# Performance work log

Hardware: AMD Instinct MI355X
Metric: run time of the kernel (lower is better)

Reference implementation:

```python
import jax, jax.numpy as jnp
import numpy as np

D = 256
H = 16
HD = D // H
N_BIAS = 6
B, E = 8, 1024


def _layernorm(x, g, b, eps=1e-5):
    mu = jnp.mean(x, axis=-1, keepdims=True)
    var = jnp.mean(jnp.square(x - mu), axis=-1, keepdims=True)
    return (x - mu) * jax.lax.rsqrt(var + eps) * g + b


def setup_inputs() -> dict:
    key = jax.random.key(0)
    ks = jax.random.split(key, 16)
    s = 0.02
    inp = {
        "x": jax.random.normal(ks[0], (B, E, D), dtype=jnp.float32),
        "struct_bias": jax.random.randint(ks[1], (B, E, E), 0, N_BIAS),
        "key_padding_mask": jnp.zeros((B, E), dtype=bool),
        # projections stored as [in, out] so y = x @ W + b
        "Wq": jax.random.normal(ks[2], (D, D), jnp.float32) * s,
        "bq": jnp.zeros((D,), jnp.float32),
        "Wk": jax.random.normal(ks[3], (D, D), jnp.float32) * s,
        "bk": jnp.zeros((D,), jnp.float32),
        "Wv": jax.random.normal(ks[4], (D, D), jnp.float32) * s,
        "bv": jnp.zeros((D,), jnp.float32),
        "Wo": jax.random.normal(ks[5], (D, D), jnp.float32) * s,
        "bo": jnp.zeros((D,), jnp.float32),
        "bias_emb": jax.random.normal(ks[6], (N_BIAS, H), jnp.float32) * s,
        "ln1_g": jnp.ones((D,), jnp.float32),
        "ln1_b": jnp.zeros((D,), jnp.float32),
        "W_ff1": jax.random.normal(ks[7], (D, 4 * D), jnp.float32) * s,
        "b_ff1": jnp.zeros((4 * D,), jnp.float32),
        "W_ff2": jax.random.normal(ks[8], (4 * D, D), jnp.float32) * s,
        "b_ff2": jnp.zeros((D,), jnp.float32),
        "ln2_g": jnp.ones((D,), jnp.float32),
        "ln2_b": jnp.zeros((D,), jnp.float32),
    }
    return inp


def reference(x, struct_bias, key_padding_mask, Wq, bq, Wk, bk, Wv, bv, Wo, bo,
              bias_emb, ln1_g, ln1_b, W_ff1, b_ff1, W_ff2, b_ff2, ln2_g, ln2_b):
    b, e, d = x.shape
    # project and split heads: [B, H, E, HD]
    q = (x @ Wq + bq).reshape(b, e, H, HD).transpose(0, 2, 1, 3)
    k = (x @ Wk + bk).reshape(b, e, H, HD).transpose(0, 2, 1, 3)
    v = (x @ Wv + bv).reshape(b, e, H, HD).transpose(0, 2, 1, 3)
    scores = jnp.einsum('bhqd,bhkd->bhqk', q, k) / np.sqrt(HD).astype(np.float32)
    # learned structural bias: [B,E,E,H] -> [B,H,E,E]
    bias = bias_emb[struct_bias].transpose(0, 3, 1, 2)
    scores = scores + bias
    scores = jnp.where(key_padding_mask[:, None, None, :], -jnp.inf, scores)
    attn = jax.nn.softmax(scores, axis=-1)
    out = jnp.einsum('bhqk,bhkd->bhqd', attn, v)
    out = out.transpose(0, 2, 1, 3).reshape(b, e, d)
    out = out @ Wo + bo
    x = _layernorm(x + out, ln1_g, ln1_b)
    ff = jax.nn.gelu(x @ W_ff1 + b_ff1, approximate=False) @ W_ff2 + b_ff2
    x = _layernorm(x + ff, ln2_g, ln2_b)
    return x
```

## Files before the change

### kernel.cpp

```cpp
#include <hip/hip_runtime.h>
#include <math.h>

#define B_  8
#define E_  1024
#define D_  256
#define H_  16
#define FF_ 1024
#define M_  (B_ * E_)

typedef __attribute__((ext_vector_type(8))) short short8;
typedef __attribute__((ext_vector_type(4))) float f32x4;
typedef unsigned short bf16u;

#define GLOAD_LDS16(g, l) __builtin_amdgcn_global_load_lds( \
    (const __attribute__((address_space(1))) void*)(g), \
    (__attribute__((address_space(3))) void*)(l), 16, 0, 0)

__device__ __forceinline__ unsigned short f2bf(float f) {
  union { float f; unsigned u; } c; c.f = f;
  unsigned r = c.u + 0x7fffu + ((c.u >> 16) & 1u);
  return (unsigned short)(r >> 16);
}
__device__ __forceinline__ float gelu_exact(float x) {
  return 0.5f * x * (1.0f + erff(x * 0.70710678118654752f));
}

template<int BM, int BN, int EPI>
__global__ __launch_bounds__(256) void mm_k(
    const bf16u* __restrict__ A, const bf16u* __restrict__ Wt,
    const float* __restrict__ bias, const float* __restrict__ R,
    void* __restrict__ Cout, int M, int N, int K)
{
  constexpr int WM = BM / 2, WN = BN / 2;
  constexpr int MT = WM / 16, NT = WN / 16;
  constexpr int PA = BM * 8 / 256, PB = BN * 8 / 256;
  constexpr int LBM = (BM == 128 ? 7 : 6), LBN = (BN == 128 ? 7 : 6);
  __shared__ bf16u As[BM * 64];
  __shared__ bf16u Bs[BN * 64];

  const int t = threadIdx.x;
  const int l15 = t & 15, quad = (t >> 4) & 3;
  const int w = t >> 6, wm = w >> 1, wn = w & 1;
  const int m0 = blockIdx.x * BM, n0 = blockIdx.y * BN;

  f32x4 acc[MT][NT];
  const f32x4 z4 = {0.f, 0.f, 0.f, 0.f};
#pragma unroll
  for (int i = 0; i < MT; ++i)
#pragma unroll
    for (int j = 0; j < NT; ++j) acc[i][j] = z4;

  for (int k0 = 0; k0 < K; k0 += 64) {
    __syncthreads();
#pragma unroll
    for (int p = 0; p < PA; ++p) {
      int g = p * 256 + t;
      int m = g & (BM - 1), c = g >> LBM;
      const bf16u* src = A + (size_t)(m0 + m) * K + k0 + c * 8;
      GLOAD_LDS16(src, As + g * 8);
    }
#pragma unroll
    for (int p = 0; p < PB; ++p) {
      int g = p * 256 + t;
      int n = g & (BN - 1), c = g >> LBN;
      const bf16u* src = Wt + (size_t)(n0 + n) * K + k0 + c * 8;
      GLOAD_LDS16(src, Bs + g * 8);
    }
    __syncthreads();
#pragma unroll
    for (int s = 0; s < 2; ++s) {
      short8 af[MT], bfr[NT];
#pragma unroll
      for (int mt = 0; mt < MT; ++mt)
        af[mt] = *(const short8*)(As + ((s * 4 + quad) * BM + wm * WM + mt * 16 + l15) * 8);
#pragma unroll
      for (int nt = 0; nt < NT; ++nt)
        bfr[nt] = *(const short8*)(Bs + ((s * 4 + quad) * BN + wn * WN + nt * 16 + l15) * 8);
#pragma unroll
      for (int mt = 0; mt < MT; ++mt)
#pragma unroll
        for (int nt = 0; nt < NT; ++nt)
          acc[mt][nt] = __builtin_amdgcn_mfma_f32_16x16x32_bf16(
              af[mt], bfr[nt], acc[mt][nt], 0, 0, 0);
    }
  }

#pragma unroll
  for (int mt = 0; mt < MT; ++mt) {
#pragma unroll
    for (int nt = 0; nt < NT; ++nt) {
      int col = n0 + wn * WN + nt * 16 + l15;
      float bia = bias[col];
#pragma unroll
      for (int r = 0; r < 4; ++r) {
        int row = m0 + wm * WM + mt * 16 + quad * 4 + r;
        float v = acc[mt][nt][r] + bia;
        if (EPI == 3) {
          size_t pidx = ((((size_t)(row >> 10) * 16 + ((col >> 4) & 15)) * 3 +
                          (col >> 8)) * E_ + (row & 1023)) * 16 + (col & 15);
          ((bf16u*)Cout)[pidx] = f2bf(v);
        } else {
          size_t idx = (size_t)row * N + col;
          if (EPI == 1)      { ((float*)Cout)[idx] = v + R[idx]; }
          else if (EPI == 2) { ((bf16u*)Cout)[idx] = f2bf(gelu_exact(v)); }
          else               { ((bf16u*)Cout)[idx] = f2bf(v); }
        }
      }
    }
  }
}

__global__ __launch_bounds__(256) void prep_k(
    const float* __restrict__ Wq, const float* __restrict__ Wk,
    const float* __restrict__ Wv, const float* __restrict__ Wo,
    const float* __restrict__ Wf1, const float* __restrict__ Wf2,
    bf16u* __restrict__ Wqkvt, bf16u* __restrict__ Wot,
    bf16u* __restrict__ Wf1t, bf16u* __restrict__ Wf2t,
    const float* __restrict__ bq, const float* __restrict__ bk,
    const float* __restrict__ bv, float* __restrict__ bqkv,
    const float* __restrict__ X, bf16u* __restrict__ Xb)
{
  __shared__ float tile[32][33];
  const int gid = blockIdx.x;
  const int t = threadIdx.x;

  if (gid < 768) {
    const float* src; bf16u* dst; int K, N, bx, by;
    if (gid < 256) {
      const int z = gid >> 6, r = gid & 63;
      src = (z == 0) ? Wq : (z == 1) ? Wk : (z == 2) ? Wv : Wo;
      dst = (z == 0) ? Wqkvt : (z == 1) ? Wqkvt + 65536
          : (z == 2) ? Wqkvt + 131072 : Wot;
      K = 256; N = 256; bx = r & 7; by = r >> 3;
    } else if (gid < 512) {
      const int r = gid - 256;
      src = Wf1; dst = Wf1t; K = 256; N = 1024; bx = r & 7; by = r >> 3;
    } else {
      const int r = gid - 512;
      src = Wf2; dst = Wf2t; K = 1024; N = 256; bx = r & 31; by = r >> 5;
    }
    const int tx = t & 31, ty = t >> 5;
    const int kb = bx * 32, nb = by * 32;
#pragma unroll
    for (int r = 0; r < 4; ++r)
      tile[ty + 8 * r][tx] = src[(size_t)(kb + ty + 8 * r) * N + nb + tx];
    __syncthreads();
#pragma unroll
    for (int r = 0; r < 4; ++r)
      dst[(size_t)(nb + ty + 8 * r) * K + kb + tx] = f2bf(tile[tx][ty + 8 * r]);
  } else if (gid < 771) {
    int i = (gid - 768) * 256 + t;
    bqkv[i] = (i < 256) ? bq[i] : (i < 512) ? bk[i - 256] : bv[i - 512];
  } else {
    int i = (gid - 771) * 256 + t;
    float4 a = ((const float4*)X)[i * 2];
    float4 b = ((const float4*)X)[i * 2 + 1];
    uint4 o;
    o.x = f2bf(a.x) | ((unsigned)f2bf(a.y) << 16);
    o.y = f2bf(a.z) | ((unsigned)f2bf(a.w) << 16);
    o.z = f2bf(b.x) | ((unsigned)f2bf(b.y) << 16);
    o.w = f2bf(b.z) | ((unsigned)f2bf(b.w) << 16);
    ((uint4*)Xb)[i] = o;
  }
}

__global__ __launch_bounds__(256) void attn_k(
    const bf16u* __restrict__ qkv, const int* __restrict__ sb,
    const unsigned char* __restrict__ mask, const float* __restrict__ be,
    bf16u* __restrict__ O)
{
  __shared__ bf16u Kl[2][2][64][40];
  __shared__ bf16u Vt[2][2][2][16][40];
  __shared__ float emb2[6][2];

  const int t    = threadIdx.x;
  const int b    = blockIdx.z;
  const int hg   = blockIdx.y;
  const int w    = t >> 6;
  const int lane = t & 63;
  const int l15  = lane & 15;
  const int quad = lane >> 4;
  const int q0w  = blockIdx.x * 64 + w * 16;
  const float C2 = 0.36067376022224085f;

  if (t < 12) emb2[t >> 1][t & 1] = be[(t >> 1) * 16 + hg * 2 + (t & 1)] * 1.44269504088896f;

  {
    float4 z = {0.f, 0.f, 0.f, 0.f};
    float4* kp = (float4*)&Kl[0][0][0][0];
    for (int i = t; i < 1280; i += 256) kp[i] = z;
  }

  short8 qf[2];
#pragma unroll
  for (int hp = 0; hp < 2; ++hp) {
    uint4 v = {0u, 0u, 0u, 0u};
    if (quad < 2)
      v = *(const uint4*)(qkv +
          ((((size_t)b * 16 + hg * 2 + hp) * 3 + 0) * E_ + q0w + l15) * 16 + quad * 8);
    else if (quad == 2)
      v.x = 0x3F80u;
    union { uint4 u; short8 s; } c; c.u = v;
    qf[hp] = c.s;
  }

  const int s_hp   = t >> 7;
  const int s_key  = (t >> 1) & 63;
  const int s_half = t & 1;
  const int vu     = t & 127;
  const int vz     = vu >> 2;
  const int vh     = (vu >> 1) & 1;
  const int vjh    = vu & 1;
  const int vs2    = vz >> 4;
  const int vrow0  = vh * 8 + vjh * 4;
  const int vc     = ((vz >> 1) & 3) * 8 + ((vz >> 3) & 1) * 4 + (vz & 1) * 2;

  const bf16u* kbase = qkv + (((size_t)b * 16 + hg * 2 + s_hp) * 3 + 1) * E_ * 16 + s_half * 8;
  const bf16u* vbase = qkv + (((size_t)b * 16 + hg * 2 + s_hp) * 3 + 2) * E_ * 16 + vrow0;
  const int* sbp = sb + ((size_t)(b * E_) + q0w + l15) * E_;

  f32x4 accO[2];
  const f32x4 z4 = {0.f, 0.f, 0.f, 0.f};
  accO[0] = z4; accO[1] = z4;
  float lsum[2] = {0.f, 0.f};

  uint4 kA;
  uint2 va, vb;
  unsigned mA;
  int sraw[2][2][4];
  {
    kA = *(const uint4*)(kbase + (size_t)s_key * 16);
    const bf16u* p0 = vbase + (size_t)(2 * vz) * 16;
    va = *(const uint2*)p0;
    vb = *(const uint2*)(p0 + 16);
    mA = mask[b * E_ + s_key];
#pragma unroll
    for (int s2 = 0; s2 < 2; ++s2)
#pragma unroll
      for (int kb2 = 0; kb2 < 2; ++kb2)
        *(int4*)&sraw[s2][kb2][0] =
            *(const int4*)(sbp + s2 * 32 + kb2 * 16 + quad * 4);
  }
  __syncthreads();

#pragma unroll 2
  for (int i = 0; i < 16; ++i) {
    const int cur = i & 1;

    *(uint4*)&Kl[cur][s_hp][s_key][s_half * 8] = kA;
    {
      union { uint2 u; bf16u e[4]; } a, c; a.u = va; c.u = vb;
#pragma unroll
      for (int j = 0; j < 4; ++j)
        *(unsigned*)&Vt[cur][s_hp][vs2][vrow0 + j][vc] =
            (unsigned)a.e[j] | ((unsigned)c.e[j] << 16);
    }
    if (s_half == 0)
      Kl[cur][s_hp][s_key][16] = mA ? (bf16u)0xCF6E : (bf16u)0;

    __syncthreads();

    int srn[2][2][4];
    if (i < 15) {
      const int kn = (i + 1) * 64;
      kA = *(const uint4*)(kbase + (size_t)(kn + s_key) * 16);
      const bf16u* p0 = vbase + (size_t)(kn + 2 * vz) * 16;
      va = *(const uint2*)p0;
      vb = *(const uint2*)(p0 + 16);
      mA = mask[b * E_ + kn + s_key];
#pragma unroll
      for (int s2 = 0; s2 < 2; ++s2)
#pragma unroll
        for (int kb2 = 0; kb2 < 2; ++kb2)
          *(int4*)&srn[s2][kb2][0] =
              *(const int4*)(sbp + kn + s2 * 32 + kb2 * 16 + quad * 4);
    }

#pragma unroll
    for (int s2 = 0; s2 < 2; ++s2) {
      short8 k00 = *(const short8*)&Kl[cur][0][s2 * 32 + l15][quad * 8];
      short8 k01 = *(const short8*)&Kl[cur][0][s2 * 32 + 16 + l15][quad * 8];
      short8 k10 = *(const short8*)&Kl[cur][1][s2 * 32 + l15][quad * 8];
      short8 k11 = *(const short8*)&Kl[cur][1][s2 * 32 + 16 + l15][quad * 8];
      f32x4 sc00 = __builtin_amdgcn_mfma_f32_16x16x32_bf16(k00, qf[0], z4, 0, 0, 0);
      f32x4 sc01 = __builtin_amdgcn_mfma_f32_16x16x32_bf16(k01, qf[0], z4, 0, 0, 0);
      f32x4 sc10 = __builtin_amdgcn_mfma_f32_16x16x32_bf16(k10, qf[1], z4, 0, 0, 0);
      f32x4 sc11 = __builtin_amdgcn_mfma_f32_16x16x32_bf16(k11, qf[1], z4, 0, 0, 0);

      unsigned pk0[4], pk1[4];
#pragma unroll
      for (int r = 0; r < 4; ++r) {
        float2 w0 = *(const float2*)&emb2[sraw[s2][0][r]][0];
        float2 w1 = *(const float2*)&emb2[sraw[s2][1][r]][0];
        float p00 = __builtin_amdgcn_exp2f(fmaf(sc00[r], C2, w0.x));
        float p01 = __builtin_amdgcn_exp2f(fmaf(sc01[r], C2, w1.x));
        float p10 = __builtin_amdgcn_exp2f(fmaf(sc10[r], C2, w0.y));
        float p11 = __builtin_amdgcn_exp2f(fmaf(sc11[r], C2, w1.y));
        unsigned u00 = __float_as_uint(p00), u01 = __float_as_uint(p01);
        unsigned u10 = __float_as_uint(p10), u11 = __float_as_uint(p11);
        lsum[0] += __uint_as_float(u00 & 0xffff0000u) + __uint_as_float(u01 & 0xffff0000u);
        lsum[1] += __uint_as_float(u10 & 0xffff0000u) + __uint_as_float(u11 & 0xffff0000u);
        if ((r & 1) == 0) {
          pk0[r >> 1]       = u00 >> 16;
          pk0[2 + (r >> 1)] = u01 >> 16;
          pk1[r >> 1]       = u10 >> 16;
          pk1[2 + (r >> 1)] = u11 >> 16;
        } else {
          pk0[r >> 1]       |= u00 & 0xffff0000u;
          pk0[2 + (r >> 1)] |= u01 & 0xffff0000u;
          pk1[r >> 1]       |= u10 & 0xffff0000u;
          pk1[2 + (r >> 1)] |= u11 & 0xffff0000u;
        }
      }
      union { unsigned u[4]; short8 s; } a0, a1;
      a0.u[0] = pk0[0]; a0.u[1] = pk0[1]; a0.u[2] = pk0[2]; a0.u[3] = pk0[3];
      a1.u[0] = pk1[0]; a1.u[1] = pk1[1]; a1.u[2] = pk1[2]; a1.u[3] = pk1[3];

      short8 vf0 = *(const short8*)&Vt[cur][0][s2][l15][quad * 8];
      short8 vf1 = *(const short8*)&Vt[cur][1][s2][l15][quad * 8];
      accO[0] = __builtin_amdgcn_mfma_f32_16x16x32_bf16(a0.s, vf0, accO[0], 0, 0, 0);
      accO[1] = __builtin_amdgcn_mfma_f32_16x16x32_bf16(a1.s, vf1, accO[1], 0, 0, 0);
    }

    if (i < 15) {
#pragma unroll
      for (int s2 = 0; s2 < 2; ++s2)
#pragma unroll
        for (int kb2 = 0; kb2 < 2; ++kb2)
#pragma unroll
          for (int r = 0; r < 4; ++r)
            sraw[s2][kb2][r] = srn[s2][kb2][r];
    }
  }

#pragma unroll
  for (int hp = 0; hp < 2; ++hp) {
    lsum[hp] += __shfl_xor(lsum[hp], 16, 64);
    lsum[hp] += __shfl_xor(lsum[hp], 32, 64);
  }
#pragma unroll
  for (int hp = 0; hp < 2; ++hp) {
#pragma unroll
    for (int r = 0; r < 4; ++r) {
      float lq = __shfl(lsum[hp], quad * 4 + r, 64);
      float o = accO[hp][r] / lq;
      O[((size_t)(b * E_) + q0w + quad * 4 + r) * 256 + (hg * 2 + hp) * 16 + l15] = f2bf(o);
    }
  }
}

template<int DUAL>
__global__ __launch_bounds__(256) void ln_k(
    const float* __restrict__ X, const float* __restrict__ g,
    const float* __restrict__ bta, float* __restrict__ Y, bf16u* __restrict__ Yb)
{
  const int row  = blockIdx.x * 4 + (threadIdx.x >> 6);
  const int lane = threadIdx.x & 63;
  float4 v = *(const float4*)(X + (size_t)row * D_ + lane * 4);
  float s  = v.x + v.y + v.z + v.w;
  float ss = v.x * v.x + v.y * v.y + v.z * v.z + v.w * v.w;
#pragma unroll
  for (int off = 32; off; off >>= 1) {
    s  += __shfl_xor(s, off, 64);
    ss += __shfl_xor(ss, off, 64);
  }
  float mu  = s * (1.f / 256.f);
  float var = ss * (1.f / 256.f) - mu * mu;
  float rs  = 1.f / sqrtf(var + 1e-5f);
  float4 gv = *(const float4*)(g + lane * 4);
  float4 bv = *(const float4*)(bta + lane * 4);
  float4 o;
  o.x = (v.x - mu) * rs * gv.x + bv.x;
  o.y = (v.y - mu) * rs * gv.y + bv.y;
  o.z = (v.z - mu) * rs * gv.z + bv.z;
  o.w = (v.w - mu) * rs * gv.w + bv.w;
  *(float4*)(Y + (size_t)row * D_ + lane * 4) = o;
  if (DUAL) {
    uint2 p;
    p.x = f2bf(o.x) | ((unsigned)f2bf(o.y) << 16);
    p.y = f2bf(o.z) | ((unsigned)f2bf(o.w) << 16);
    *(uint2*)(Yb + (size_t)row * D_ + lane * 4) = p;
  }
}

extern "C" void kernel_launch(void* const* d_in, const int* in_sizes, int n_in,
                              void* d_out, int out_size, void* d_ws, size_t ws_size,
                              hipStream_t stream) {
  const float* x   = (const float*)d_in[0];
  const int*   sb  = (const int*)d_in[1];
  const unsigned char* mask = (const unsigned char*)d_in[2];
  const float* Wq  = (const float*)d_in[3];
  const float* bq  = (const float*)d_in[4];
  const float* Wk  = (const float*)d_in[5];
  const float* bk  = (const float*)d_in[6];
  const float* Wv  = (const float*)d_in[7];
  const float* bv  = (const float*)d_in[8];
  const float* Wo  = (const float*)d_in[9];
  const float* bo  = (const float*)d_in[10];
  const float* be  = (const float*)d_in[11];
  const float* g1  = (const float*)d_in[12];
  const float* b1  = (const float*)d_in[13];
  const float* Wf1 = (const float*)d_in[14];
  const float* bf1 = (const float*)d_in[15];
  const float* Wf2 = (const float*)d_in[16];
  const float* bf2 = (const float*)d_in[17];
  const float* g2  = (const float*)d_in[18];
  const float* b2  = (const float*)d_in[19];
  float* out = (float*)d_out;

  char* ws = (char*)d_ws;
  bf16u* Wqkvt = (bf16u*)(ws + 0);
  bf16u* Wot   = (bf16u*)(ws + 393216);
  bf16u* Wf1t  = (bf16u*)(ws + 524288);
  bf16u* Wf2t  = (bf16u*)(ws + 1048576);
  float* bqkv  = (float*)(ws + 1572864);
  bf16u* xb    = (bf16u*)(ws + 2097152);
  bf16u* qkv   = (bf16u*)(ws + 6291456);
  bf16u* att   = (bf16u*)(ws + 18874368);
  float* t1    = (float*)(ws + 23068672);
  float* x1    = (float*)(ws + 31457280);
  bf16u* x1b   = (bf16u*)(ws + 39845888);
  bf16u* ffh   = (bf16u*)(ws + 2097152);
  float* t2    = (float*)(ws + 18874368);

  dim3 blk(256);

  prep_k<<<1795, blk, 0, stream>>>(Wq, Wk, Wv, Wo, Wf1, Wf2,
                                   Wqkvt, Wot, Wf1t, Wf2t,
                                   bq, bk, bv, bqkv, x, xb);

  mm_k<64, 128, 3><<<dim3(128, 6), blk, 0, stream>>>(xb, Wqkvt, bqkv, nullptr,
                                                     qkv, M_, 768, 256);
  attn_k<<<dim3(16, 8, 8), blk, 0, stream>>>(qkv, sb, mask, be, att);

  mm_k<64, 64, 1><<<dim3(128, 4), blk, 0, stream>>>(att, Wot, bo, x,
                                                    t1, M_, 256, 256);
  ln_k<1><<<M_ / 4, blk, 0, stream>>>(t1, g1, b1, x1, x1b);

  mm_k<128, 128, 2><<<dim3(64, 8), blk, 0, stream>>>(x1b, Wf1t, bf1, nullptr,
                                                     ffh, M_, 1024, 256);
  mm_k<64, 64, 1><<<dim3(128, 4), blk, 0, stream>>>(ffh, Wf2t, bf2, x1,
                                                    t2, M_, 256, 1024);
  ln_k<0><<<M_ / 4, blk, 0, stream>>>(t2, g2, b2, out, nullptr);
}
```

Measured before the change: 230.2 us.

## Process two query sub-tiles per wave in attention to reuse K/V tiles

Each wave now handles 32 query rows (two 16-row sub-tiles) instead of 16, so each block covers 128 queries and the grid is halved. The K/V tiles staged in shared memory and the LDS fragment reads are reused across both sub-tiles, which halves the K/V global loads and staging work per query. In exchange, register pressure roughly doubles for accumulators and prefetched struct-bias indices, and only 512 blocks are launched, which may lower occupancy and latency hiding.

```diff
diff --git a/kernel.cpp b/kernel.cpp
--- a/kernel.cpp
+++ b/kernel.cpp
@@ -180,7 +180,7 @@
   const int lane = t & 63;
   const int l15  = lane & 15;
   const int quad = lane >> 4;
-  const int q0w  = blockIdx.x * 64 + w * 16;
+  const int q0w  = blockIdx.x * 128 + w * 32;
   const float C2 = 0.36067376022224085f;
 
   if (t < 12) emb2[t >> 1][t & 1] = be[(t >> 1) * 16 + hg * 2 + (t & 1)] * 1.44269504088896f;
@@ -191,18 +191,20 @@
     for (int i = t; i < 1280; i += 256) kp[i] = z;
   }
 
-  short8 qf[2];
-#pragma unroll
-  for (int hp = 0; hp < 2; ++hp) {
-    uint4 v = {0u, 0u, 0u, 0u};
-    if (quad < 2)
-      v = *(const uint4*)(qkv +
-          ((((size_t)b * 16 + hg * 2 + hp) * 3 + 0) * E_ + q0w + l15) * 16 + quad * 8);
-    else if (quad == 2)
-      v.x = 0x3F80u;
-    union { uint4 u; short8 s; } c; c.u = v;
-    qf[hp] = c.s;
-  }
+  short8 qf[2][2];
+#pragma unroll
+  for (int sub = 0; sub < 2; ++sub)
+#pragma unroll
+    for (int hp = 0; hp < 2; ++hp) {
+      uint4 v = {0u, 0u, 0u, 0u};
+      if (quad < 2)
+        v = *(const uint4*)(qkv +
+            ((((size_t)b * 16 + hg * 2 + hp) * 3 + 0) * E_ + q0w + sub * 16 + l15) * 16 + quad * 8);
+      else if (quad == 2)
+        v.x = 0x3F80u;
+      union { uint4 u; short8 s; } c; c.u = v;
+      qf[sub][hp] = c.s;
+    }
 
   const int s_hp   = t >> 7;
   const int s_key  = (t >> 1) & 63;
@@ -217,17 +219,18 @@
 
   const bf16u* kbase = qkv + (((size_t)b * 16 + hg * 2 + s_hp) * 3 + 1) * E_ * 16 + s_half * 8;
   const bf16u* vbase = qkv + (((size_t)b * 16 + hg * 2 + s_hp) * 3 + 2) * E_ * 16 + vrow0;
-  const int* sbp = sb + ((size_t)(b * E_) + q0w + l15) * E_;
-
-  f32x4 accO[2];
+  const int* sbp0 = sb + ((size_t)(b * E_) + q0w + l15) * E_;
+  const int* sbp1 = sb + ((size_t)(b * E_) + q0w + 16 + l15) * E_;
+
+  f32x4 accO[2][2];
   const f32x4 z4 = {0.f, 0.f, 0.f, 0.f};
-  accO[0] = z4; accO[1] = z4;
-  float lsum[2] = {0.f, 0.f};
+  accO[0][0] = z4; accO[0][1] = z4; accO[1][0] = z4; accO[1][1] = z4;
+  float lsum[2][2] = {{0.f, 0.f}, {0.f, 0.f}};
 
   uint4 kA;
   uint2 va, vb;
   unsigned mA;
-  int sraw[2][2][4];
+  int sraw[2][2][2][4];
   {
     kA = *(const uint4*)(kbase + (size_t)s_key * 16);
     const bf16u* p0 = vbase + (size_t)(2 * vz) * 16;
@@ -237,9 +240,12 @@
 #pragma unroll
     for (int s2 = 0; s2 < 2; ++s2)
 #pragma unroll
-      for (int kb2 = 0; kb2 < 2; ++kb2)
-        *(int4*)&sraw[s2][kb2][0] =
-            *(const int4*)(sbp + s2 * 32 + kb2 * 16 + quad * 4);
+      for (int kb2 = 0; kb2 < 2; ++kb2) {
+        *(int4*)&sraw[0][s2][kb2][0] =
+            *(const int4*)(sbp0 + s2 * 32 + kb2 * 16 + quad * 4);
+        *(int4*)&sraw[1][s2][kb2][0] =
+            *(const int4*)(sbp1 + s2 * 32 + kb2 * 16 + quad * 4);
+      }
   }
   __syncthreads();
 
@@ -260,7 +266,7 @@
 
     __syncthreads();
 
-    int srn[2][2][4];
+    int srn[2][2][2][4];
     if (i < 15) {
       const int kn = (i + 1) * 64;
       kA = *(const uint4*)(kbase + (size_t)(kn + s_key) * 16);
@@ -271,9 +277,12 @@
 #pragma unroll
       for (int s2 = 0; s2 < 2; ++s2)
 #pragma unroll
-        for (int kb2 = 0; kb2 < 2; ++kb2)
-          *(int4*)&srn[s2][kb2][0] =
-              *(const int4*)(sbp + kn + s2 * 32 + kb2 * 16 + quad * 4);
+        for (int kb2 = 0; kb2 < 2; ++kb2) {
+          *(int4*)&srn[0][s2][kb2][0] =
+              *(const int4*)(sbp0 + kn + s2 * 32 + kb2 * 16 + quad * 4);
+          *(int4*)&srn[1][s2][kb2][0] =
+              *(const int4*)(sbp1 + kn + s2 * 32 + kb2 * 16 + quad * 4);
+        }
     }
 
 #pragma unroll
@@ -282,71 +291,81 @@
       short8 k01 = *(const short8*)&Kl[cur][0][s2 * 32 + 16 + l15][quad * 8];
       short8 k10 = *(const short8*)&Kl[cur][1][s2 * 32 + l15][quad * 8];
       short8 k11 = *(const short8*)&Kl[cur][1][s2 * 32 + 16 + l15][quad * 8];
-      f32x4 sc00 = __builtin_amdgcn_mfma_f32_16x16x32_bf16(k00, qf[0], z4, 0, 0, 0);
-      f32x4 sc01 = __builtin_amdgcn_mfma_f32_16x16x32_bf16(k01, qf[0], z4, 0, 0, 0);
-      f32x4 sc10 = __builtin_amdgcn_mfma_f32_16x16x32_bf16(k10, qf[1], z4, 0, 0, 0);
-      f32x4 sc11 = __builtin_amdgcn_mfma_f32_16x16x32_bf16(k11, qf[1], z4, 0, 0, 0);
-
-      unsigned pk0[4], pk1[4];
-#pragma unroll
-      for (int r = 0; r < 4; ++r) {
-        float2 w0 = *(const float2*)&emb2[sraw[s2][0][r]][0];
-        float2 w1 = *(const float2*)&emb2[sraw[s2][1][r]][0];
-        float p00 = __builtin_amdgcn_exp2f(fmaf(sc00[r], C2, w0.x));
-        float p01 = __builtin_amdgcn_exp2f(fmaf(sc01[r], C2, w1.x));
-        float p10 = __builtin_amdgcn_exp2f(fmaf(sc10[r], C2, w0.y));
-        float p11 = __builtin_amdgcn_exp2f(fmaf(sc11[r], C2, w1.y));
-        unsigned u00 = __float_as_uint(p00), u01 = __float_as_uint(p01);
-        unsigned u10 = __float_as_uint(p10), u11 = __float_as_uint(p11);
-        lsum[0] += __uint_as_float(u00 & 0xffff0000u) + __uint_as_float(u01 & 0xffff0000u);
-        lsum[1] += __uint_as_float(u10 & 0xffff0000u) + __uint_as_float(u11 & 0xffff0000u);
-        if ((r & 1) == 0) {
-          pk0[r >> 1]       = u00 >> 16;
-          pk0[2 + (r >> 1)] = u01 >> 16;
-          pk1[r >> 1]       = u10 >> 16;
-          pk1[2 + (r >> 1)] = u11 >> 16;
-        } else {
-          pk0[r >> 1]       |= u00 & 0xffff0000u;
-          pk0[2 + (r >> 1)] |= u01 & 0xffff0000u;
-          pk1[r >> 1]       |= u10 & 0xffff0000u;
-          pk1[2 + (r >> 1)] |= u11 & 0xffff0000u;
-        }
-      }
-      union { unsigned u[4]; short8 s; } a0, a1;
-      a0.u[0] = pk0[0]; a0.u[1] = pk0[1]; a0.u[2] = pk0[2]; a0.u[3] = pk0[3];
-      a1.u[0] = pk1[0]; a1.u[1] = pk1[1]; a1.u[2] = pk1[2]; a1.u[3] = pk1[3];
-
       short8 vf0 = *(const short8*)&Vt[cur][0][s2][l15][quad * 8];
       short8 vf1 = *(const short8*)&Vt[cur][1][s2][l15][quad * 8];
-      accO[0] = __builtin_amdgcn_mfma_f32_16x16x32_bf16(a0.s, vf0, accO[0], 0, 0, 0);
-      accO[1] = __builtin_amdgcn_mfma_f32_16x16x32_bf16(a1.s, vf1, accO[1], 0, 0, 0);
+#pragma unroll
+      for (int sub = 0; sub < 2; ++sub) {
+        f32x4 sc00 = __builtin_amdgcn_mfma_f32_16x16x32_bf16(k00, qf[sub][0], z4, 0, 0, 0);
+        f32x4 sc01 = __builtin_amdgcn_mfma_f32_16x16x32_bf16(k01, qf[sub][0], z4, 0, 0, 0);
+        f32x4 sc10 = __builtin_amdgcn_mfma_f32_16x16x32_bf16(k10, qf[sub][1], z4, 0, 0, 0);
+        f32x4 sc11 = __builtin_amdgcn_mfma_f32_16x16x32_bf16(k11, qf[sub][1], z4, 0, 0, 0);
+
+        unsigned pk0[4], pk1[4];
+#pragma unroll
+        for (int r = 0; r < 4; ++r) {
+          float2 w0 = *(const float2*)&emb2[sraw[sub][s2][0][r]][0];
+          float2 w1 = *(const float2*)&emb2[sraw[sub][s2][1][r]][0];
+          float p00 = __builtin_amdgcn_exp2f(fmaf(sc00[r], C2, w0.x));
+          float p01 = __builtin_amdgcn_exp2f(fmaf(sc01[r], C2, w1.x));
+          float p10 = __builtin_amdgcn_exp2f(fmaf(sc10[r], C2, w0.y));
+          float p11 = __builtin_amdgcn_exp2f(fmaf(sc11[r], C2, w1.y));
+          unsigned u00 = __float_as_uint(p00), u01 = __float_as_uint(p01);
+          unsigned u10 = __float_as_uint(p10), u11 = __float_as_uint(p11);
+          lsum[sub][0] += __uint_as_float(u00 & 0xffff0000u) + __uint_as_float(u01 & 0xffff0000u);
+          lsum[sub][1] += __uint_as_float(u10 & 0xffff0000u) + __uint_as_float(u11 & 0xffff0000u);
+          if ((r & 1) == 0) {
+            pk0[r >> 1]       = u00 >> 16;
+            pk0[2 + (r >> 1)] = u01 >> 16;
+            pk1[r >> 1]       = u10 >> 16;
+            pk1[2 + (r >> 1)] = u11 >> 16;
+          } else {
+            pk0[r >> 1]       |= u00 & 0xffff0000u;
+            pk0[2 + (r >> 1)] |= u01 & 0xffff0000u;
+            pk1[r >> 1]       |= u10 & 0xffff0000u;
+            pk1[2 + (r >> 1)] |= u11 & 0xffff0000u;
+          }
+        }
+        union { unsigned u[4]; short8 s; } a0, a1;
+        a0.u[0] = pk0[0]; a0.u[1] = pk0[1]; a0.u[2] = pk0[2]; a0.u[3] = pk0[3];
+        a1.u[0] = pk1[0]; a1.u[1] = pk1[1]; a1.u[2] = pk1[2]; a1.u[3] = pk1[3];
+
+        accO[sub][0] = __builtin_amdgcn_mfma_f32_16x16x32_bf16(a0.s, vf0, accO[sub][0], 0, 0, 0);
+        accO[sub][1] = __builtin_amdgcn_mfma_f32_16x16x32_bf16(a1.s, vf1, accO[sub][1], 0, 0, 0);
+      }
     }
 
     if (i < 15) {
 #pragma unroll
-      for (int s2 = 0; s2 < 2; ++s2)
-#pragma unroll
-        for (int kb2 = 0; kb2 < 2; ++kb2)
-#pragma unroll
-          for (int r = 0; r < 4; ++r)
-            sraw[s2][kb2][r] = srn[s2][kb2][r];
-    }
-  }
-
-#pragma unroll
-  for (int hp = 0; hp < 2; ++hp) {
-    lsum[hp] += __shfl_xor(lsum[hp], 16, 64);
-    lsum[hp] += __shfl_xor(lsum[hp], 32, 64);
-  }
-#pragma unroll
-  for (int hp = 0; hp < 2; ++hp) {
-#pragma unroll
-    for (int r = 0; r < 4; ++r) {
-      float lq = __shfl(lsum[hp], quad * 4 + r, 64);
-      float o = accO[hp][r] / lq;
-      O[((size_t)(b * E_) + q0w + quad * 4 + r) * 256 + (hg * 2 + hp) * 16 + l15] = f2bf(o);
-    }
-  }
+      for (int sub = 0; sub < 2; ++sub)
+#pragma unroll
+        for (int s2 = 0; s2 < 2; ++s2)
+#pragma unroll
+          for (int kb2 = 0; kb2 < 2; ++kb2)
+#pragma unroll
+            for (int r = 0; r < 4; ++r)
+              sraw[sub][s2][kb2][r] = srn[sub][s2][kb2][r];
+    }
+  }
+
+#pragma unroll
+  for (int sub = 0; sub < 2; ++sub)
+#pragma unroll
+    for (int hp = 0; hp < 2; ++hp) {
+      lsum[sub][hp] += __shfl_xor(lsum[sub][hp], 16, 64);
+      lsum[sub][hp] += __shfl_xor(lsum[sub][hp], 32, 64);
+    }
+#pragma unroll
+  for (int sub = 0; sub < 2; ++sub)
+#pragma unroll
+    for (int hp = 0; hp < 2; ++hp) {
+#pragma unroll
+      for (int r = 0; r < 4; ++r) {
+        float lq = __shfl(lsum[sub][hp], quad * 4 + r, 64);
+        float o = accO[sub][hp][r] / lq;
+        O[((size_t)(b * E_) + q0w + sub * 16 + quad * 4 + r) * 256 +
+          (hg * 2 + hp) * 16 + l15] = f2bf(o);
+      }
+    }
 }
 
 template<int DUAL>
@@ -431,7 +450,7 @@
 
   mm_k<64, 128, 3><<<dim3(128, 6), blk, 0, stream>>>(xb, Wqkvt, bqkv, nullptr,
                                                      qkv, M_, 768, 256);
-  attn_k<<<dim3(16, 8, 8), blk, 0, stream>>>(qkv, sb, mask, be, att);
+  attn_k<<<dim3(8, 8, 8), blk, 0, stream>>>(qkv, sb, mask, be, att);
 
   mm_k<64, 64, 1><<<dim3(128, 4), blk, 0, stream>>>(att, Wot, bo, x,
                                                     t1, M_, 256, 256);
```

Result: slower. 249.5 us (+8.4%).
